# Optimization experiments

Hardware: AMD Instinct MI355X
Metric: run time of the kernel (lower is better)

The kernel has to match this reference:

```python
import jax, jax.numpy as jnp
import numpy as np
import math

D_MODEL = 256
N_LEVELS = 4
N_HEADS = 8
N_POINTS = 4
SPATIAL = [[92, 160], [46, 80], [23, 40], [12, 20]]  # (H_l, W_l)
BATCH = 8
LEN_Q = 8192


def setup_inputs() -> dict:
    key = jax.random.key(0)
    ks = jax.random.split(key, 8)
    len_in = sum(h * w for h, w in SPATIAL)
    query = jax.random.normal(ks[0], (BATCH, LEN_Q, D_MODEL), jnp.float32)
    reference_points = jax.random.uniform(ks[1], (BATCH, LEN_Q, N_LEVELS, 2), jnp.float32)
    input_flatten = jax.random.normal(ks[2], (BATCH, len_in, D_MODEL), jnp.float32)
    input_spatial_shapes = jnp.array(SPATIAL, jnp.int32)
    starts = np.cumsum([0] + [h * w for h, w in SPATIAL])[:-1]
    input_level_start_index = jnp.array(starts, jnp.int32)
    # learned params (sampling_offsets bias uses the directional grid init from _reset_parameters)
    W_off = jax.random.normal(ks[3], (D_MODEL, N_HEADS * N_LEVELS * N_POINTS * 2), jnp.float32) * 0.01
    thetas = jnp.arange(N_HEADS, dtype=jnp.float32) * (2.0 * math.pi / N_HEADS)
    grid = jnp.stack([jnp.cos(thetas), jnp.sin(thetas)], -1)
    grid = grid / jnp.max(jnp.abs(grid), axis=-1, keepdims=True)
    grid = jnp.tile(grid[:, None, None, :], (1, N_LEVELS, N_POINTS, 1))
    grid = grid * jnp.arange(1, N_POINTS + 1, dtype=jnp.float32)[None, None, :, None]
    b_off = grid.reshape(-1)
    W_attn = jax.random.normal(ks[4], (D_MODEL, N_HEADS * N_LEVELS * N_POINTS), jnp.float32) * 0.02
    b_attn = jnp.zeros((N_HEADS * N_LEVELS * N_POINTS,), jnp.float32)
    W_val = jax.random.normal(ks[5], (D_MODEL, D_MODEL), jnp.float32) * (1.0 / math.sqrt(D_MODEL))
    b_val = jnp.zeros((D_MODEL,), jnp.float32)
    W_out = jax.random.normal(ks[6], (D_MODEL, D_MODEL), jnp.float32) * (1.0 / math.sqrt(D_MODEL))
    b_out = jnp.zeros((D_MODEL,), jnp.float32)
    return dict(query=query, reference_points=reference_points, input_flatten=input_flatten,
                input_spatial_shapes=input_spatial_shapes,
                input_level_start_index=input_level_start_index,
                W_off=W_off, b_off=b_off, W_attn=W_attn, b_attn=b_attn,
                W_val=W_val, b_val=b_val, W_out=W_out, b_out=b_out)


def _ms_deform_attn(query, reference_points, input_flatten, spatial_shapes_np,
                    W_off, b_off, W_attn, b_attn, W_val, b_val, W_out, b_out):
    Nb, Lq, C = query.shape
    Hh, L, P = N_HEADS, N_LEVELS, N_POINTS
    Dh = C // Hh
    value = (input_flatten @ W_val + b_val).reshape(Nb, -1, Hh, Dh)
    attn = (query @ W_attn + b_attn).reshape(Nb, Lq, Hh, L * P)
    attn = jax.nn.softmax(attn, axis=-1).reshape(Nb, Lq, Hh, L, P)
    off = (query @ W_off + b_off).reshape(Nb, Lq, Hh, L, P, 2)
    # offset_normalizer = (W_l, H_l)
    norm = jnp.asarray(np.stack([spatial_shapes_np[:, 1], spatial_shapes_np[:, 0]], -1),
                       dtype=query.dtype)  # (L, 2)
    loc = reference_points[:, :, None, :, None, :] + off / norm[None, None, None, :, None, :]
    out = jnp.zeros((Nb, Lq, Hh, Dh), query.dtype)
    start = 0
    for l in range(L):
        H, W = int(spatial_shapes_np[l, 0]), int(spatial_shapes_np[l, 1])
        v = value[:, start:start + H * W]                       # (Nb, H*W, Hh, Dh)
        start += H * W
        v = v.transpose(0, 2, 1, 3).reshape(Nb * Hh, H * W, Dh)  # (B2, H*W, Dh)
        g = loc[:, :, :, l].transpose(0, 2, 1, 3, 4).reshape(Nb * Hh, Lq * P, 2)
        # grid_sample with grid = 2*loc-1, align_corners=False, zero padding
        x = g[..., 0] * W - 0.5
        y = g[..., 1] * H - 0.5
        x0f = jnp.floor(x); y0f = jnp.floor(y)
        wx = x - x0f; wy = y - y0f
        x0 = x0f.astype(jnp.int32); y0 = y0f.astype(jnp.int32)

        def gather(xi, yi):
            valid = (xi >= 0) & (xi < W) & (yi >= 0) & (yi < H)
            idx = jnp.clip(yi, 0, H - 1) * W + jnp.clip(xi, 0, W - 1)
            samp = jnp.take_along_axis(v, idx[..., None], axis=1)  # (B2, Lq*P, Dh)
            return samp * valid[..., None].astype(v.dtype)

        s = (gather(x0, y0) * ((1 - wx) * (1 - wy))[..., None]
             + gather(x0 + 1, y0) * (wx * (1 - wy))[..., None]
             + gather(x0, y0 + 1) * ((1 - wx) * wy)[..., None]
             + gather(x0 + 1, y0 + 1) * (wx * wy)[..., None])
        s = s.reshape(Nb, Hh, Lq, P, Dh)
        w = attn[:, :, :, l].transpose(0, 2, 1, 3)  # (Nb, Hh, Lq, P)
        out = out + jnp.einsum('bhqp,bhqpd->bqhd', w, s)
    return out.reshape(Nb, Lq, C) @ W_out + b_out


def reference(query, reference_points, input_flatten, input_spatial_shapes,
              input_level_start_index, W_off, b_off, W_attn, b_attn,
              W_val, b_val, W_out, b_out):
    # spatial shapes are static metadata (define per-level view sizes)
    shapes_np = np.asarray(input_spatial_shapes)
    del input_level_start_index  # levels are contiguous; starts derived from shapes
    return _ms_deform_attn(query, reference_points, input_flatten, shapes_np,
                           W_off, b_off, W_attn, b_attn, W_val, b_val, W_out, b_out)
```

## Files before the change

### kernel.cpp

```cpp
#include <hip/hip_runtime.h>
#include <hip/hip_bf16.h>
#include <cstddef>
#include <cstdint>

#define NB 8
#define LQ 8192
#define DMODEL 256
#define NHD 8
#define NLV 4
#define NPT 4
#define LEN_IN 19560
#define NQ (NB * LQ)
#define MV (NB * LEN_IN)
#define MVP 156544

using bf16x8 = __attribute__((ext_vector_type(8))) short;
using f32x4  = __attribute__((ext_vector_type(4))) float;

typedef const __attribute__((address_space(1))) void* gas_ptr;
typedef __attribute__((address_space(3))) void* las_ptr;

__device__ __forceinline__ void gl_lds16(const void* g, void* l) {
  __builtin_amdgcn_global_load_lds((gas_ptr)g, (las_ptr)l, 16, 0, 0);
}
__device__ __forceinline__ float bflo(unsigned u) {
  union { unsigned i; float f; } c; c.i = u << 16; return c.f;
}
__device__ __forceinline__ float bfhi(unsigned u) {
  union { unsigned i; float f; } c; c.i = u & 0xffff0000u; return c.f;
}

__global__ __launch_bounds__(256) void convert_bf16_pad(
    const float* __restrict__ src, __hip_bfloat16* __restrict__ dst,
    long src_elems) {
  const long idx8 = (long)(blockIdx.x * 256 + threadIdx.x) * 8;
  ushort4 o0, o1;
  if (idx8 < src_elems) {
    float4 f0 = *(const float4*)(src + idx8);
    float4 f1 = *(const float4*)(src + idx8 + 4);
    o0 = {__bfloat16_as_ushort(__float2bfloat16(f0.x)),
          __bfloat16_as_ushort(__float2bfloat16(f0.y)),
          __bfloat16_as_ushort(__float2bfloat16(f0.z)),
          __bfloat16_as_ushort(__float2bfloat16(f0.w))};
    o1 = {__bfloat16_as_ushort(__float2bfloat16(f1.x)),
          __bfloat16_as_ushort(__float2bfloat16(f1.y)),
          __bfloat16_as_ushort(__float2bfloat16(f1.z)),
          __bfloat16_as_ushort(__float2bfloat16(f1.w))};
  } else {
    o0 = {0, 0, 0, 0};
    o1 = {0, 0, 0, 0};
  }
  *(ushort4*)((unsigned short*)dst + idx8) = o0;
  *(ushort4*)((unsigned short*)dst + idx8 + 4) = o1;
}

__global__ __launch_bounds__(256) void transpose_bf16(
    const float* __restrict__ W, __hip_bfloat16* __restrict__ Bt, int N) {
  const int o = blockIdx.x * 256 + threadIdx.x;
  const int n = o >> 8, k = o & 255;
  Bt[o] = __float2bfloat16(W[(size_t)k * N + n]);
}

template <int OUT_MODE>
__global__ __launch_bounds__(256) void gemm_mfma(
    const __hip_bfloat16* __restrict__ A, const __hip_bfloat16* __restrict__ Bt,
    const float* __restrict__ bias, void* __restrict__ Cout, int N,
    int M_valid) {
  __shared__ __hip_bfloat16 As[128 * 32];
  __shared__ __hip_bfloat16 Bs[128 * 32];

  const int tid = threadIdx.x;
  const int wv = tid >> 6;
  const int lane = tid & 63;
  const int quad = lane >> 4;
  const int l16 = lane & 15;
  const int bm = blockIdx.y * 128;
  const int bn = blockIdx.x * 128;
  const int rw = (wv & 1) * 64;
  const int cw = (wv >> 1) * 64;

  const __hip_bfloat16* gA = A + (size_t)(bm + (tid >> 2)) * 256 + (tid & 3) * 8;
  const __hip_bfloat16* gB = Bt + (size_t)(bn + (tid >> 2)) * 256 + (tid & 3) * 8;
  char* ldsA0 = (char*)As + wv * 1024;
  char* ldsB0 = (char*)Bs + wv * 1024;

  f32x4 acc[4][4] = {};

#pragma unroll 1
  for (int k0 = 0; k0 < 256; k0 += 32) {
    __syncthreads();
    gl_lds16(gA + k0, ldsA0);
    gl_lds16(gA + 64 * 256 + k0, ldsA0 + 4096);
    gl_lds16(gB + k0, ldsB0);
    gl_lds16(gB + 64 * 256 + k0, ldsB0 + 4096);
    __syncthreads();

    bf16x8 af[4], bfr[4];
#pragma unroll
    for (int t = 0; t < 4; ++t) {
      af[t] = *(const bf16x8*)(As + (rw + t * 16 + l16) * 32 + quad * 8);
      bfr[t] = *(const bf16x8*)(Bs + (cw + t * 16 + l16) * 32 + quad * 8);
    }
#pragma unroll
    for (int i = 0; i < 4; ++i)
#pragma unroll
      for (int j = 0; j < 4; ++j)
        acc[i][j] = __builtin_amdgcn_mfma_f32_16x16x32_bf16(af[i], bfr[j],
                                                            acc[i][j], 0, 0, 0);
  }

#pragma unroll
  for (int j = 0; j < 4; ++j) {
    const int col = bn + cw + j * 16 + l16;
    const float bb = bias[col];
#pragma unroll
    for (int i = 0; i < 4; ++i) {
#pragma unroll
      for (int r = 0; r < 4; ++r) {
        const int row = bm + rw + i * 16 + quad * 4 + r;
        const float v = acc[i][j][r] + bb;
        if (OUT_MODE == 0) {
          ((float*)Cout)[(size_t)row * N + col] = v;
        } else if (OUT_MODE == 1) {
          ((__hip_bfloat16*)Cout)[(size_t)row * N + col] = __float2bfloat16(v);
        } else {
          if (row < M_valid) {
            const int b = row / LEN_IN;
            const int pix = row - b * LEN_IN;
            const int h = col >> 5, ch = col & 31;
            ((__hip_bfloat16*)Cout)[(((size_t)(b * 8 + h) * LEN_IN + pix) << 5) +
                                    ch] = __float2bfloat16(v);
          }
        }
      }
    }
  }
}

__global__ __launch_bounds__(256) void msda_sample4(
    const float* __restrict__ refp,
    const float* __restrict__ logits,
    const __hip_bfloat16* __restrict__ offb,
    const __hip_bfloat16* __restrict__ vh,
    __hip_bfloat16* __restrict__ mid) {
  const int q0 = blockIdx.x * 2;
  const int tid = threadIdx.x;

  __shared__ int2 s_d[2][8][17][4];

  {
    const int sq = tid >> 7;
    const int t = tid & 127;
    const int qg = q0 + sq;
    const int l = (t >> 2) & 3;
    constexpr int Hs[4] = {92, 46, 23, 12};
    constexpr int Ws_[4] = {160, 80, 40, 20};
    constexpr int St[4] = {0, 14720, 18400, 19320};
    const int Hl = Hs[l], Wl = Ws_[l];

    const float lg = logits[(size_t)qg * 128 + t];
    float mx = lg;
#pragma unroll
    for (int d = 1; d < 16; d <<= 1) mx = fmaxf(mx, __shfl_xor(mx, d));
    const float e = expf(lg - mx);
    float sm = e;
#pragma unroll
    for (int d = 1; d < 16; d <<= 1) sm += __shfl_xor(sm, d);
    const float w = e / sm;

    const float rx = refp[(size_t)qg * 8 + 2 * l];
    const float ry = refp[(size_t)qg * 8 + 2 * l + 1];
    const unsigned uo = *(const unsigned*)(offb + (size_t)qg * 256 + 2 * t);
    const float ox = bflo(uo), oy = bfhi(uo);

    const float x = rx * (float)Wl + ox - 0.5f;
    const float y = ry * (float)Hl + oy - 0.5f;
    const float xf = floorf(x), yf = floorf(y);
    const float wx = x - xf, wy = y - yf;
    const int x0 = (int)xf, y0 = (int)yf;
    const int x1 = x0 + 1, y1 = y0 + 1;
    const bool vx0 = (x0 >= 0) & (x0 < Wl), vx1 = (x1 >= 0) & (x1 < Wl);
    const bool vy0 = (y0 >= 0) & (y0 < Hl), vy1 = (y1 >= 0) & (y1 < Hl);
    const int cx0 = min(max(x0, 0), Wl - 1), cx1 = min(max(x1, 0), Wl - 1);
    const int cy0 = min(max(y0, 0), Hl - 1), cy1 = min(max(y1, 0), Hl - 1);

    const int o00 = (St[l] + cy0 * Wl + cx0) * 64;
    const int o01 = (St[l] + cy1 * Wl + cx0) * 64;
    const int dx = (cx1 - cx0) * 64;

    int2* dd = s_d[sq][t >> 4][t & 15];
    dd[0] = make_int2(o00,      __float_as_int((vx0 & vy0) ? w * (1.f - wx) * (1.f - wy) : 0.f));
    dd[1] = make_int2(o00 + dx, __float_as_int((vx1 & vy0) ? w * wx * (1.f - wy) : 0.f));
    dd[2] = make_int2(o01,      __float_as_int((vx0 & vy1) ? w * (1.f - wx) * wy : 0.f));
    dd[3] = make_int2(o01 + dx, __float_as_int((vx1 & vy1) ? w * wx * wy : 0.f));
  }
  __syncthreads();

  const int tap = tid & 3;
  const int cg = (tid >> 2) & 3;
  const int h = (tid >> 4) & 7;
  const int sq = tid >> 7;
  const int qg = q0 + sq;
  const int bq = q0 >> 13;

  const char* vbase = (const char*)vh + (size_t)bq * (8ULL * LEN_IN * 64);
  const int voff0 = h * (LEN_IN * 64) + cg * 16;
  const int2* sd = &s_d[sq][h][0][tap];

  float a[8] = {};
#pragma unroll
  for (int pt = 0; pt < 16; ++pt) {
    const int2 dw = sd[pt * 4];
    const float w = __int_as_float(dw.y);
    const unsigned voff = (unsigned)(voff0 + dw.x);
    const uint4 u = *(const uint4*)(vbase + voff);
    a[0] += w * bflo(u.x); a[1] += w * bfhi(u.x);
    a[2] += w * bflo(u.y); a[3] += w * bfhi(u.y);
    a[4] += w * bflo(u.z); a[5] += w * bfhi(u.z);
    a[6] += w * bflo(u.w); a[7] += w * bfhi(u.w);
  }

#pragma unroll
  for (int i = 0; i < 8; ++i) a[i] += __shfl_xor(a[i], 1);
#pragma unroll
  for (int i = 0; i < 8; ++i) a[i] += __shfl_xor(a[i], 2);

  if (tap == 0) {
    unsigned short* mp =
        (unsigned short*)mid + (size_t)qg * 256 + h * 32 + cg * 8;
    int4 o;
    o.x = (int)((unsigned)__bfloat16_as_ushort(__float2bfloat16(a[0])) |
                ((unsigned)__bfloat16_as_ushort(__float2bfloat16(a[1])) << 16));
    o.y = (int)((unsigned)__bfloat16_as_ushort(__float2bfloat16(a[2])) |
                ((unsigned)__bfloat16_as_ushort(__float2bfloat16(a[3])) << 16));
    o.z = (int)((unsigned)__bfloat16_as_ushort(__float2bfloat16(a[4])) |
                ((unsigned)__bfloat16_as_ushort(__float2bfloat16(a[5])) << 16));
    o.w = (int)((unsigned)__bfloat16_as_ushort(__float2bfloat16(a[6])) |
                ((unsigned)__bfloat16_as_ushort(__float2bfloat16(a[7])) << 16));
    *(int4*)mp = o;
  }
}

extern "C" void kernel_launch(void* const* d_in, const int* in_sizes, int n_in,
                              void* d_out, int out_size, void* d_ws,
                              size_t ws_size, hipStream_t stream) {
  const float* query = (const float*)d_in[0];
  const float* refp = (const float*)d_in[1];
  const float* inflat = (const float*)d_in[2];
  const float* W_off = (const float*)d_in[5];
  const float* b_off = (const float*)d_in[6];
  const float* W_attn = (const float*)d_in[7];
  const float* b_attn = (const float*)d_in[8];
  const float* W_val = (const float*)d_in[9];
  const float* b_val = (const float*)d_in[10];
  const float* W_out = (const float*)d_in[11];
  const float* b_out = (const float*)d_in[12];
  float* out = (float*)d_out;

  char* ws = (char*)d_ws;
  __hip_bfloat16* Abuf = (__hip_bfloat16*)(ws);
  __hip_bfloat16* Qbuf = (__hip_bfloat16*)(ws + 80150528ULL);
  __hip_bfloat16* vh = (__hip_bfloat16*)(ws + 113704960ULL);
  float* logits = (float*)(ws + 193822720ULL);
  __hip_bfloat16* offb = (__hip_bfloat16*)(ws + 227377152ULL);
  __hip_bfloat16* mid = (__hip_bfloat16*)(ws + 260931584ULL);
  __hip_bfloat16* Btv = (__hip_bfloat16*)(ws + 294486016ULL);
  __hip_bfloat16* Bta = (__hip_bfloat16*)(ws + 294617088ULL);
  __hip_bfloat16* Bto = (__hip_bfloat16*)(ws + 294682624ULL);
  __hip_bfloat16* Btw = (__hip_bfloat16*)(ws + 294813696ULL);

  convert_bf16_pad<<<(MVP * 256 / 8) / 256, 256, 0, stream>>>(
      inflat, Abuf, (long)MV * 256);
  convert_bf16_pad<<<(NQ * 256 / 8) / 256, 256, 0, stream>>>(
      query, Qbuf, (long)NQ * 256);
  transpose_bf16<<<256, 256, 0, stream>>>(W_val, Btv, 256);
  transpose_bf16<<<128, 256, 0, stream>>>(W_attn, Bta, 128);
  transpose_bf16<<<256, 256, 0, stream>>>(W_off, Bto, 256);
  transpose_bf16<<<256, 256, 0, stream>>>(W_out, Btw, 256);

  gemm_mfma<2><<<dim3(2, MVP / 128), 256, 0, stream>>>(Abuf, Btv, b_val, vh,
                                                       256, MV);
  gemm_mfma<0><<<dim3(1, NQ / 128), 256, 0, stream>>>(Qbuf, Bta, b_attn,
                                                      logits, 128, NQ);
  gemm_mfma<1><<<dim3(2, NQ / 128), 256, 0, stream>>>(Qbuf, Bto, b_off, offb,
                                                      256, NQ);
  msda_sample4<<<NQ / 2, 256, 0, stream>>>(refp, logits, offb, vh, mid);
  gemm_mfma<0><<<dim3(2, NQ / 128), 256, 0, stream>>>(mid, Btw, b_out, out,
                                                      256, NQ);
}
```

Baseline: 596.9 us.

## Fuse fp32-to-bf16 conversion into GEMM loads and merge attn/offset GEMMs

```diff
diff --git a/kernel.cpp b/kernel.cpp
--- a/kernel.cpp
+++ b/kernel.cpp
@@ -29,29 +29,17 @@
 __device__ __forceinline__ float bfhi(unsigned u) {
   union { unsigned i; float f; } c; c.i = u & 0xffff0000u; return c.f;
 }
-
-__global__ __launch_bounds__(256) void convert_bf16_pad(
-    const float* __restrict__ src, __hip_bfloat16* __restrict__ dst,
-    long src_elems) {
-  const long idx8 = (long)(blockIdx.x * 256 + threadIdx.x) * 8;
-  ushort4 o0, o1;
-  if (idx8 < src_elems) {
-    float4 f0 = *(const float4*)(src + idx8);
-    float4 f1 = *(const float4*)(src + idx8 + 4);
-    o0 = {__bfloat16_as_ushort(__float2bfloat16(f0.x)),
-          __bfloat16_as_ushort(__float2bfloat16(f0.y)),
-          __bfloat16_as_ushort(__float2bfloat16(f0.z)),
-          __bfloat16_as_ushort(__float2bfloat16(f0.w))};
-    o1 = {__bfloat16_as_ushort(__float2bfloat16(f1.x)),
-          __bfloat16_as_ushort(__float2bfloat16(f1.y)),
-          __bfloat16_as_ushort(__float2bfloat16(f1.z)),
-          __bfloat16_as_ushort(__float2bfloat16(f1.w))};
-  } else {
-    o0 = {0, 0, 0, 0};
-    o1 = {0, 0, 0, 0};
-  }
-  *(ushort4*)((unsigned short*)dst + idx8) = o0;
-  *(ushort4*)((unsigned short*)dst + idx8 + 4) = o1;
+__device__ __forceinline__ bf16x8 pack8(float4 a, float4 b) {
+  bf16x8 o;
+  o[0] = (short)__bfloat16_as_ushort(__float2bfloat16(a.x));
+  o[1] = (short)__bfloat16_as_ushort(__float2bfloat16(a.y));
+  o[2] = (short)__bfloat16_as_ushort(__float2bfloat16(a.z));
+  o[3] = (short)__bfloat16_as_ushort(__float2bfloat16(a.w));
+  o[4] = (short)__bfloat16_as_ushort(__float2bfloat16(b.x));
+  o[5] = (short)__bfloat16_as_ushort(__float2bfloat16(b.y));
+  o[6] = (short)__bfloat16_as_ushort(__float2bfloat16(b.z));
+  o[7] = (short)__bfloat16_as_ushort(__float2bfloat16(b.w));
+  return o;
 }
 
 __global__ __launch_bounds__(256) void transpose_bf16(
@@ -61,11 +49,11 @@
   Bt[o] = __float2bfloat16(W[(size_t)k * N + n]);
 }
 
-template <int OUT_MODE>
+template <int OUT_MODE, int A_F32>
 __global__ __launch_bounds__(256) void gemm_mfma(
-    const __hip_bfloat16* __restrict__ A, const __hip_bfloat16* __restrict__ Bt,
-    const float* __restrict__ bias, void* __restrict__ Cout, int N,
-    int M_valid) {
+    const void* __restrict__ Av, const __hip_bfloat16* __restrict__ Bt,
+    const float* __restrict__ bias, const float* __restrict__ bias2,
+    void* __restrict__ Cout, void* __restrict__ Cout2, int N, int M_valid) {
   __shared__ __hip_bfloat16 As[128 * 32];
   __shared__ __hip_bfloat16 Bs[128 * 32];
 
@@ -79,20 +67,49 @@
   const int rw = (wv & 1) * 64;
   const int cw = (wv >> 1) * 64;
 
-  const __hip_bfloat16* gA = A + (size_t)(bm + (tid >> 2)) * 256 + (tid & 3) * 8;
   const __hip_bfloat16* gB = Bt + (size_t)(bn + (tid >> 2)) * 256 + (tid & 3) * 8;
+  char* ldsB0 = (char*)Bs + wv * 1024;
+
+  const __hip_bfloat16* gA16 = nullptr;
+  const float* gA32 = nullptr;
   char* ldsA0 = (char*)As + wv * 1024;
-  char* ldsB0 = (char*)Bs + wv * 1024;
+  __hip_bfloat16* dA = nullptr;
+  bool okA = true;
+  if (A_F32) {
+    const int r = tid >> 1, half = tid & 1;
+    okA = (bm + r) < M_valid;
+    gA32 = (const float*)Av + (size_t)(bm + r) * 256 + half * 16;
+    dA = As + r * 32 + half * 16;
+  } else {
+    gA16 = (const __hip_bfloat16*)Av + (size_t)(bm + (tid >> 2)) * 256 +
+           (tid & 3) * 8;
+  }
 
   f32x4 acc[4][4] = {};
 
 #pragma unroll 1
   for (int k0 = 0; k0 < 256; k0 += 32) {
+    float4 f0, f1, f2, f3;
+    if (A_F32) {
+      if (okA) {
+        f0 = *(const float4*)(gA32 + k0);
+        f1 = *(const float4*)(gA32 + k0 + 4);
+        f2 = *(const float4*)(gA32 + k0 + 8);
+        f3 = *(const float4*)(gA32 + k0 + 12);
+      } else {
+        f0 = f1 = f2 = f3 = make_float4(0.f, 0.f, 0.f, 0.f);
+      }
+    }
     __syncthreads();
-    gl_lds16(gA + k0, ldsA0);
-    gl_lds16(gA + 64 * 256 + k0, ldsA0 + 4096);
     gl_lds16(gB + k0, ldsB0);
     gl_lds16(gB + 64 * 256 + k0, ldsB0 + 4096);
+    if (A_F32) {
+      *(bf16x8*)dA = pack8(f0, f1);
+      *(bf16x8*)(dA + 8) = pack8(f2, f3);
+    } else {
+      gl_lds16(gA16 + k0, ldsA0);
+      gl_lds16(gA16 + 64 * 256 + k0, ldsA0 + 4096);
+    }
     __syncthreads();
 
     bf16x8 af[4], bfr[4];
@@ -112,7 +129,11 @@
 #pragma unroll
   for (int j = 0; j < 4; ++j) {
     const int col = bn + cw + j * 16 + l16;
-    const float bb = bias[col];
+    float bb;
+    if (OUT_MODE == 3)
+      bb = (bn == 0) ? bias[col] : bias2[col - 128];
+    else
+      bb = bias[col];
 #pragma unroll
     for (int i = 0; i < 4; ++i) {
 #pragma unroll
@@ -121,15 +142,20 @@
         const float v = acc[i][j][r] + bb;
         if (OUT_MODE == 0) {
           ((float*)Cout)[(size_t)row * N + col] = v;
-        } else if (OUT_MODE == 1) {
-          ((__hip_bfloat16*)Cout)[(size_t)row * N + col] = __float2bfloat16(v);
-        } else {
+        } else if (OUT_MODE == 2) {
           if (row < M_valid) {
             const int b = row / LEN_IN;
             const int pix = row - b * LEN_IN;
             const int h = col >> 5, ch = col & 31;
             ((__hip_bfloat16*)Cout)[(((size_t)(b * 8 + h) * LEN_IN + pix) << 5) +
                                     ch] = __float2bfloat16(v);
+          }
+        } else {
+          if (bn == 0) {
+            ((float*)Cout)[(size_t)row * 128 + col] = v;
+          } else {
+            ((__hip_bfloat16*)Cout2)[(size_t)row * 256 + (col - 128)] =
+                __float2bfloat16(v);
           }
         }
       }
@@ -258,33 +284,24 @@
   float* out = (float*)d_out;
 
   char* ws = (char*)d_ws;
-  __hip_bfloat16* Abuf = (__hip_bfloat16*)(ws);
-  __hip_bfloat16* Qbuf = (__hip_bfloat16*)(ws + 80150528ULL);
-  __hip_bfloat16* vh = (__hip_bfloat16*)(ws + 113704960ULL);
-  float* logits = (float*)(ws + 193822720ULL);
-  __hip_bfloat16* offb = (__hip_bfloat16*)(ws + 227377152ULL);
-  __hip_bfloat16* mid = (__hip_bfloat16*)(ws + 260931584ULL);
-  __hip_bfloat16* Btv = (__hip_bfloat16*)(ws + 294486016ULL);
-  __hip_bfloat16* Bta = (__hip_bfloat16*)(ws + 294617088ULL);
-  __hip_bfloat16* Bto = (__hip_bfloat16*)(ws + 294682624ULL);
-  __hip_bfloat16* Btw = (__hip_bfloat16*)(ws + 294813696ULL);
-
-  convert_bf16_pad<<<(MVP * 256 / 8) / 256, 256, 0, stream>>>(
-      inflat, Abuf, (long)MV * 256);
-  convert_bf16_pad<<<(NQ * 256 / 8) / 256, 256, 0, stream>>>(
-      query, Qbuf, (long)NQ * 256);
+  __hip_bfloat16* vh = (__hip_bfloat16*)(ws);
+  float* logits = (float*)(ws + 80117760ULL);
+  __hip_bfloat16* offb = (__hip_bfloat16*)(ws + 113672192ULL);
+  __hip_bfloat16* mid = (__hip_bfloat16*)(ws + 147226624ULL);
+  __hip_bfloat16* Btv = (__hip_bfloat16*)(ws + 180781056ULL);
+  __hip_bfloat16* Btc = (__hip_bfloat16*)(ws + 180912128ULL);
+  __hip_bfloat16* Btw = (__hip_bfloat16*)(ws + 181108736ULL);
+
   transpose_bf16<<<256, 256, 0, stream>>>(W_val, Btv, 256);
-  transpose_bf16<<<128, 256, 0, stream>>>(W_attn, Bta, 128);
-  transpose_bf16<<<256, 256, 0, stream>>>(W_off, Bto, 256);
+  transpose_bf16<<<128, 256, 0, stream>>>(W_attn, Btc, 128);
+  transpose_bf16<<<256, 256, 0, stream>>>(W_off, Btc + 128 * 256, 256);
   transpose_bf16<<<256, 256, 0, stream>>>(W_out, Btw, 256);
 
-  gemm_mfma<2><<<dim3(2, MVP / 128), 256, 0, stream>>>(Abuf, Btv, b_val, vh,
-                                                       256, MV);
-  gemm_mfma<0><<<dim3(1, NQ / 128), 256, 0, stream>>>(Qbuf, Bta, b_attn,
-                                                      logits, 128, NQ);
-  gemm_mfma<1><<<dim3(2, NQ / 128), 256, 0, stream>>>(Qbuf, Bto, b_off, offb,
-                                                      256, NQ);
+  gemm_mfma<2, 1><<<dim3(2, MVP / 128), 256, 0, stream>>>(
+      inflat, Btv, b_val, nullptr, vh, nullptr, 256, MV);
+  gemm_mfma<3, 1><<<dim3(3, NQ / 128), 256, 0, stream>>>(
+      query, Btc, b_attn, b_off, logits, offb, 384, NQ);
   msda_sample4<<<NQ / 2, 256, 0, stream>>>(refp, logits, offb, vh, mid);
-  gemm_mfma<0><<<dim3(2, NQ / 128), 256, 0, stream>>>(mid, Btw, b_out, out,
-                                                      256, NQ);
-}
+  gemm_mfma<0, 0><<<dim3(2, NQ / 128), 256, 0, stream>>>(
+      mid, Btw, b_out, nullptr, out, nullptr, 256, NQ);
+}
```

Result: faster. 575.0 us (-3.7%).
